# Kernel tuning notes

Measured on AMD Instinct MI355X. Metric: run time of the kernel, lower is better.

The kernel has to match this reference:

```python
import jax, jax.numpy as jnp
import numpy as np

B, F, INP, S = 2048, 50, 2, 1024
LN_EPS = 1e-3
UPDATE_BIAS = -1.0
_TRUNC = 0.8796256610342398  # trunc-normal std correction from weight_init


def _std(fan_in, fan_out):
    return np.sqrt(2.0 / (fan_in + fan_out)) / _TRUNC


def setup_inputs() -> dict:
    key = jax.random.key(0)
    k_act, k_emb, k_gru, k_dec = jax.random.split(key, 4)
    return {
        "action": jax.random.normal(k_act, (B, F, INP), dtype=jnp.float32),
        "W_emb": jax.random.normal(k_emb, (INP, S), dtype=jnp.float32) * _std(INP, S),
        "W_gru": jax.random.normal(k_gru, (2 * S, 3 * S), dtype=jnp.float32) * _std(2 * S, 3 * S),
        "ln_gamma": jnp.ones((3 * S,), dtype=jnp.float32),
        "ln_beta": jnp.zeros((3 * S,), dtype=jnp.float32),
        "W_dec": jax.random.normal(k_dec, (S, INP), dtype=jnp.float32) * _std(S, INP),
        "b_dec": jnp.zeros((INP,), dtype=jnp.float32),
    }


def reference(action, W_emb, W_gru, ln_gamma, ln_beta, W_dec, b_dec):
    # action: [b, f, inp]
    emb = jnp.einsum("bfi,is->bfs", action, W_emb)  # [b, f, s]

    def step(prev, x_t):
        # prev, x_t: [b, s]
        parts = jnp.concatenate([x_t, prev], axis=-1) @ W_gru  # [b, 3s]
        mu = parts.mean(-1, keepdims=True)
        var = parts.var(-1, keepdims=True)
        parts = (parts - mu) / jnp.sqrt(var + LN_EPS) * ln_gamma + ln_beta
        reset, cand, update = jnp.split(parts, 3, axis=-1)
        reset = jax.nn.sigmoid(reset)
        cand = jnp.tanh(reset * cand)
        update = jax.nn.sigmoid(update + UPDATE_BIAS)
        h = update * cand + (1.0 - update) * prev
        return h, None

    prev0 = jnp.zeros_like(emb[:, 0])
    h_last, _ = jax.lax.scan(step, prev0, jnp.swapaxes(emb, 0, 1))  # scan over f
    outputs = h_last @ W_dec + b_dec  # [b, inp]
    return h_last[:, None], outputs[:, None]
```

## Files before the change

kernel.cpp:

```cpp
#include <hip/hip_runtime.h>

typedef unsigned short u16;
typedef unsigned int   u32;
typedef _Float16       f16;

#define B_SZ 2048
#define S_SZ 1024
#define N3   3072
#define F_SZ 50

typedef f16    f16x8 __attribute__((ext_vector_type(8)));
typedef f16    f16x4 __attribute__((ext_vector_type(4)));
typedef float  f32x4 __attribute__((ext_vector_type(4)));
typedef u32    u32x4 __attribute__((ext_vector_type(4)));

__device__ __forceinline__ void glds16(const void* g, void* l) {
    __builtin_amdgcn_global_load_lds(
        (const __attribute__((address_space(1))) u32*)g,
        (__attribute__((address_space(3))) u32*)l, 16, 0, 0);
}

__global__ __launch_bounds__(256) void make_mx(
    const float* __restrict__ We, const float* __restrict__ Wg,
    float* __restrict__ Mx)
{
    int j  = blockIdx.x * 256 + threadIdx.x;
    int k0 = blockIdx.y * 64;
    float s0 = 0.f, s1 = 0.f;
    #pragma unroll 4
    for (int k = k0; k < k0 + 64; k++) {
        float w = Wg[(size_t)k * N3 + j];
        s0 += We[k] * w;
        s1 += We[S_SZ + k] * w;
    }
    atomicAdd(&Mx[j], s0);
    atomicAdd(&Mx[N3 + j], s1);
}

__global__ __launch_bounds__(256) void transpose_w(
    const float* __restrict__ Wg, f16* __restrict__ Wt)
{
    __shared__ float tile[32][33];
    int n0 = blockIdx.x * 32, k0 = blockIdx.y * 32;
    int c = threadIdx.x & 31, r = threadIdx.x >> 5;
    #pragma unroll
    for (int s = 0; s < 4; s++) {
        int rr = r + s * 8;
        tile[rr][c] = Wg[(size_t)(S_SZ + k0 + rr) * N3 + n0 + c];
    }
    __syncthreads();
    #pragma unroll
    for (int s = 0; s < 4; s++) {
        int rr = r + s * 8;
        Wt[(size_t)(n0 + rr) * S_SZ + k0 + c] = (f16)tile[c][rr];
    }
}

__global__ __launch_bounds__(256) void gemm_step(
    const f16* __restrict__ Wt,
    const f16* __restrict__ hh,
    const float* __restrict__ Mx,
    const float* __restrict__ act,
    f16* __restrict__ parts,
    int t, int m_base)
{
    __shared__ __align__(16) f16 As[64 * 64];
    __shared__ __align__(16) f16 Bs[128 * 64];
    const int m0 = m_base + blockIdx.x * 64;
    const int n0 = blockIdx.y * 128;
    const int tid  = threadIdx.x;
    const int lane = tid & 63;
    const int wave = tid >> 6;
    const int wr = (wave >> 1) * 32;
    const int wc = (wave & 1) * 64;
    const int quad = lane >> 4, lrow = lane & 15;
    const int swz = (lrow & 7) * 8;

    const int lrow8 = lane >> 3;
    const int scolh = ((lane & 7) * 8) ^ (lrow8 * 8);

    f32x4 acc[2][4];
    #pragma unroll
    for (int i = 0; i < 2; i++)
        #pragma unroll
        for (int j = 0; j < 4; j++)
            acc[i][j] = (f32x4){0.f, 0.f, 0.f, 0.f};

    for (int kb = 0; kb < S_SZ; kb += 64) {
        __syncthreads();
        #pragma unroll
        for (int c = 0; c < 2; c++) {
            int ch = wave * 2 + c;
            int row = ch * 8 + lrow8;
            glds16(&hh[(size_t)(m0 + row) * S_SZ + kb + scolh], &As[ch * 512]);
        }
        #pragma unroll
        for (int c = 0; c < 4; c++) {
            int ch = wave * 4 + c;
            int row = ch * 8 + lrow8;
            glds16(&Wt[(size_t)(n0 + row) * S_SZ + kb + scolh], &Bs[ch * 512]);
        }
        __syncthreads();
        #pragma unroll
        for (int kk = 0; kk < 64; kk += 32) {
            f16x8 a[2], b[4];
            #pragma unroll
            for (int i = 0; i < 2; i++)
                a[i] = __builtin_bit_cast(f16x8,
                    *(const u32x4*)&As[(wr + i * 16 + lrow) * 64 +
                                       ((kk + quad * 8) ^ swz)]);
            #pragma unroll
            for (int j = 0; j < 4; j++)
                b[j] = __builtin_bit_cast(f16x8,
                    *(const u32x4*)&Bs[(wc + j * 16 + lrow) * 64 +
                                       ((kk + quad * 8) ^ swz)]);
            #pragma unroll
            for (int i = 0; i < 2; i++)
                #pragma unroll
                for (int j = 0; j < 4; j++)
                    acc[i][j] = __builtin_amdgcn_mfma_f32_16x16x32_f16(
                        a[i], b[j], acc[i][j], 0, 0, 0);
        }
    }

    #pragma unroll
    for (int i = 0; i < 2; i++) {
        #pragma unroll
        for (int r = 0; r < 4; r++) {
            int m = m0 + wr + i * 16 + quad * 4 + r;
            float a0 = act[((size_t)m * F_SZ + t) * 2 + 0];
            float a1 = act[((size_t)m * F_SZ + t) * 2 + 1];
            #pragma unroll
            for (int j = 0; j < 4; j++) {
                int n = n0 + wc + j * 16 + lrow;
                parts[(size_t)(m - m_base) * N3 + n] =
                    (f16)(acc[i][j][r] + a0 * Mx[n] + a1 * Mx[N3 + n]);
            }
        }
    }
}

__global__ __launch_bounds__(256) void ln_gate_step(
    const f16* __restrict__ parts,
    const float* __restrict__ gamma,
    const float* __restrict__ beta,
    float* __restrict__ h,
    f16* __restrict__ hh,
    int m_base)
{
    const int rloc = blockIdx.x;
    const int row  = m_base + rloc;
    const int tid  = threadIdx.x;
    const f16* p = parts + (size_t)rloc * N3;
    f16x4 pr = *(const f16x4*)(p + tid * 4);
    f16x4 pc = *(const f16x4*)(p + S_SZ + tid * 4);
    f16x4 pu = *(const f16x4*)(p + 2 * S_SZ + tid * 4);
    float vr[4], vc[4], vu[4];
    float s = 0.f, ss = 0.f;
    #pragma unroll
    for (int q = 0; q < 4; q++) {
        vr[q] = (float)pr[q]; vc[q] = (float)pc[q]; vu[q] = (float)pu[q];
        s  += vr[q] + vc[q] + vu[q];
        ss += vr[q] * vr[q] + vc[q] * vc[q] + vu[q] * vu[q];
    }
    #pragma unroll
    for (int o = 32; o > 0; o >>= 1) {
        s  += __shfl_down(s, o);
        ss += __shfl_down(ss, o);
    }
    __shared__ float red[8];
    int lane = tid & 63, wave = tid >> 6;
    if (lane == 0) { red[wave] = s; red[4 + wave] = ss; }
    __syncthreads();
    float S  = red[0] + red[1] + red[2] + red[3];
    float SS = red[4] + red[5] + red[6] + red[7];
    float mean = S * (1.f / N3);
    float var  = SS * (1.f / N3) - mean * mean;
    float rstd = rsqrtf(var + 1e-3f);

    f32x4 gr = *(const f32x4*)(gamma + tid * 4);
    f32x4 gc = *(const f32x4*)(gamma + S_SZ + tid * 4);
    f32x4 gu = *(const f32x4*)(gamma + 2 * S_SZ + tid * 4);
    f32x4 br = *(const f32x4*)(beta + tid * 4);
    f32x4 bc = *(const f32x4*)(beta + S_SZ + tid * 4);
    f32x4 bu = *(const f32x4*)(beta + 2 * S_SZ + tid * 4);

    size_t hbase = (size_t)row * S_SZ + tid * 4;
    f32x4 hv = *(const f32x4*)(h + hbase);
    f32x4 hn;
    f16x4 hs;
    #pragma unroll
    for (int q = 0; q < 4; q++) {
        float nr = (vr[q] - mean) * rstd * gr[q] + br[q];
        float nc = (vc[q] - mean) * rstd * gc[q] + bc[q];
        float nu = (vu[q] - mean) * rstd * gu[q] + bu[q];
        float r = 1.f / (1.f + __expf(-nr));
        float c = tanhf(r * nc);
        float u = 1.f / (1.f + __expf(-(nu - 1.f)));
        hn[q] = u * c + (1.f - u) * hv[q];
        hs[q] = (f16)hn[q];
    }
    *(f32x4*)(h + hbase) = hn;
    *(f16x4*)(hh + hbase) = hs;
}

__global__ __launch_bounds__(256) void final_out(
    const float* __restrict__ h, const float* __restrict__ Wd,
    const float* __restrict__ bd, float* __restrict__ out)
{
    int row = blockIdx.x * 4 + (threadIdx.x >> 6);
    int lane = threadIdx.x & 63;
    const float* hr = h + (size_t)row * S_SZ;
    float s0 = 0.f, s1 = 0.f;
    #pragma unroll
    for (int k = lane; k < S_SZ; k += 64) {
        float x = hr[k];
        s0 += x * Wd[k * 2];
        s1 += x * Wd[k * 2 + 1];
    }
    #pragma unroll
    for (int o = 32; o > 0; o >>= 1) {
        s0 += __shfl_down(s0, o);
        s1 += __shfl_down(s1, o);
    }
    if (lane == 0) {
        out[(size_t)B_SZ * S_SZ + row * 2 + 0] = s0 + bd[0];
        out[(size_t)B_SZ * S_SZ + row * 2 + 1] = s1 + bd[1];
    }
}

extern "C" void kernel_launch(void* const* d_in, const int* in_sizes, int n_in,
                              void* d_out, int out_size, void* d_ws, size_t ws_size,
                              hipStream_t stream)
{
    const float* act = (const float*)d_in[0];
    const float* We  = (const float*)d_in[1];
    const float* Wg  = (const float*)d_in[2];
    const float* lng = (const float*)d_in[3];
    const float* lnb = (const float*)d_in[4];
    const float* Wd  = (const float*)d_in[5];
    const float* bd  = (const float*)d_in[6];
    float* out = (float*)d_out;
    float* h   = out;

    char* ws = (char*)d_ws;
    f16*   Wt = (f16*)ws;
    float* Mx = (float*)(ws + 6291456);
    f16*   hh = (f16*)(ws + 6316032);
    const size_t BASE = 6316032 + 4194304;
    f16* parts = (f16*)(ws + BASE);
    size_t avail = (ws_size > BASE) ? ws_size - BASE : 0;
    int rows = 2048;
    while (rows > 128 && (size_t)rows * N3 * 2 > avail) rows >>= 1;

    hipMemsetAsync(h, 0, (size_t)B_SZ * S_SZ * 4, stream);
    hipMemsetAsync(hh, 0, (size_t)B_SZ * S_SZ * 2, stream);
    hipMemsetAsync(Mx, 0, 2 * N3 * 4, stream);
    make_mx<<<dim3(N3 / 256, 16), 256, 0, stream>>>(We, Wg, Mx);
    transpose_w<<<dim3(N3 / 32, S_SZ / 32), 256, 0, stream>>>(Wg, Wt);

    for (int t = 0; t < F_SZ; t++) {
        for (int mb = 0; mb < B_SZ; mb += rows) {
            gemm_step<<<dim3(rows / 64, N3 / 128), 256, 0, stream>>>(
                Wt, hh, Mx, act, parts, t, mb);
            ln_gate_step<<<rows, 256, 0, stream>>>(parts, lng, lnb, h, hh, mb);
        }
    }
    final_out<<<B_SZ / 4, 256, 0, stream>>>(h, Wd, bd, out);
}
```

Before: 1.512 ms.

## Fuse GRU time loop into persistent cooperative kernel with per-row-block counters

```diff
diff --git a/kernel.cpp b/kernel.cpp
--- a/kernel.cpp
+++ b/kernel.cpp
@@ -2,17 +2,21 @@
 
 typedef unsigned short u16;
 typedef unsigned int   u32;
+typedef unsigned long long u64;
 typedef _Float16       f16;
 
 #define B_SZ 2048
 #define S_SZ 1024
 #define N3   3072
 #define F_SZ 50
+#define GRID 768
 
 typedef f16    f16x8 __attribute__((ext_vector_type(8)));
 typedef f16    f16x4 __attribute__((ext_vector_type(4)));
 typedef float  f32x4 __attribute__((ext_vector_type(4)));
 typedef u32    u32x4 __attribute__((ext_vector_type(4)));
+
+#define AGENT __HIP_MEMORY_SCOPE_AGENT
 
 __device__ __forceinline__ void glds16(const void* g, void* l) {
     __builtin_amdgcn_global_load_lds(
@@ -56,18 +60,27 @@
     }
 }
 
-__global__ __launch_bounds__(256) void gemm_step(
+__global__ __launch_bounds__(256, 3) void fused_loop(
     const f16* __restrict__ Wt,
-    const f16* __restrict__ hh,
+    f16* __restrict__ hh,
     const float* __restrict__ Mx,
     const float* __restrict__ act,
+    const float* __restrict__ gamma,
+    const float* __restrict__ beta,
     f16* __restrict__ parts,
-    int t, int m_base)
+    float* __restrict__ hout,
+    int* __restrict__ cnt)
 {
     __shared__ __align__(16) f16 As[64 * 64];
     __shared__ __align__(16) f16 Bs[128 * 64];
-    const int m0 = m_base + blockIdx.x * 64;
-    const int n0 = blockIdx.y * 128;
+
+    const int blk = blockIdx.x;
+    const int x8  = blk & 7;
+    const int r   = blk >> 3;
+    const int NB  = x8 * 3 + (r % 3);
+    const int M   = r / 3;
+    const int m0 = M * 64, n0 = NB * 128;
+
     const int tid  = threadIdx.x;
     const int lane = tid & 63;
     const int wave = tid >> 6;
@@ -79,129 +92,185 @@
     const int lrow8 = lane >> 3;
     const int scolh = ((lane & 7) * 8) ^ (lrow8 * 8);
 
-    f32x4 acc[2][4];
-    #pragma unroll
-    for (int i = 0; i < 2; i++)
+    const int arow = tid >> 2;
+    const int agi  = (tid & 3) * 2;
+    const int ar7  = arow & 7;
+
+    const int erow = tid >> 2;
+    const int eseg = (tid & 3) * 32;
+
+    int* gcnt = cnt + M * 16;
+    int* dcnt = cnt + 512 + M * 16;
+    const int doLN = (NB % 3) != 2;
+    const int li   = (NB / 3) * 2 + (NB % 3);
+    const int lnrow = m0 + li * 4 + wave;
+
+    float mx0[4], mx1[4];
+    #pragma unroll
+    for (int j = 0; j < 4; j++) {
+        int n = n0 + wc + j * 16 + lrow;
+        mx0[j] = Mx[n]; mx1[j] = Mx[N3 + n];
+    }
+
+    for (int t = 0; t < F_SZ; t++) {
+        if (tid == 0) {
+            int tgt = 16 * t;
+            while (__hip_atomic_load(dcnt, __ATOMIC_RELAXED, AGENT) < tgt)
+                __builtin_amdgcn_s_sleep(2);
+        }
+        __syncthreads();
+
+        f32x4 acc[2][4];
         #pragma unroll
-        for (int j = 0; j < 4; j++)
-            acc[i][j] = (f32x4){0.f, 0.f, 0.f, 0.f};
-
-    for (int kb = 0; kb < S_SZ; kb += 64) {
+        for (int i = 0; i < 2; i++)
+            #pragma unroll
+            for (int j = 0; j < 4; j++)
+                acc[i][j] = (f32x4){0.f, 0.f, 0.f, 0.f};
+
+        for (int kb = 0; kb < S_SZ; kb += 64) {
+            __syncthreads();
+            {
+                const u64* src = (const u64*)(hh + (size_t)(m0 + arow) * S_SZ + kb)
+                                 + (size_t)(tid & 3) * 4;
+                u64 d0 = __hip_atomic_load(src + 0, __ATOMIC_RELAXED, AGENT);
+                u64 d1 = __hip_atomic_load(src + 1, __ATOMIC_RELAXED, AGENT);
+                u64 d2 = __hip_atomic_load(src + 2, __ATOMIC_RELAXED, AGENT);
+                u64 d3 = __hip_atomic_load(src + 3, __ATOMIC_RELAXED, AGENT);
+                *(u64*)&As[arow * 64 + ((agi    ) ^ ar7) * 8    ] = d0;
+                *(u64*)&As[arow * 64 + ((agi    ) ^ ar7) * 8 + 4] = d1;
+                *(u64*)&As[arow * 64 + ((agi + 1) ^ ar7) * 8    ] = d2;
+                *(u64*)&As[arow * 64 + ((agi + 1) ^ ar7) * 8 + 4] = d3;
+            }
+            #pragma unroll
+            for (int c = 0; c < 4; c++) {
+                int ch = wave * 4 + c;
+                int row = ch * 8 + lrow8;
+                glds16(&Wt[(size_t)(n0 + row) * S_SZ + kb + scolh], &Bs[ch * 512]);
+            }
+            __syncthreads();
+            #pragma unroll
+            for (int kk = 0; kk < 64; kk += 32) {
+                f16x8 a[2], b[4];
+                #pragma unroll
+                for (int i = 0; i < 2; i++)
+                    a[i] = __builtin_bit_cast(f16x8,
+                        *(const u32x4*)&As[(wr + i * 16 + lrow) * 64 +
+                                           ((kk + quad * 8) ^ swz)]);
+                #pragma unroll
+                for (int j = 0; j < 4; j++)
+                    b[j] = __builtin_bit_cast(f16x8,
+                        *(const u32x4*)&Bs[(wc + j * 16 + lrow) * 64 +
+                                           ((kk + quad * 8) ^ swz)]);
+                #pragma unroll
+                for (int i = 0; i < 2; i++)
+                    #pragma unroll
+                    for (int j = 0; j < 4; j++)
+                        acc[i][j] = __builtin_amdgcn_mfma_f32_16x16x32_f16(
+                            a[i], b[j], acc[i][j], 0, 0, 0);
+            }
+        }
+
         __syncthreads();
         #pragma unroll
-        for (int c = 0; c < 2; c++) {
-            int ch = wave * 2 + c;
-            int row = ch * 8 + lrow8;
-            glds16(&hh[(size_t)(m0 + row) * S_SZ + kb + scolh], &As[ch * 512]);
-        }
-        #pragma unroll
-        for (int c = 0; c < 4; c++) {
-            int ch = wave * 4 + c;
-            int row = ch * 8 + lrow8;
-            glds16(&Wt[(size_t)(n0 + row) * S_SZ + kb + scolh], &Bs[ch * 512]);
-        }
-        __syncthreads();
-        #pragma unroll
-        for (int kk = 0; kk < 64; kk += 32) {
-            f16x8 a[2], b[4];
-            #pragma unroll
-            for (int i = 0; i < 2; i++)
-                a[i] = __builtin_bit_cast(f16x8,
-                    *(const u32x4*)&As[(wr + i * 16 + lrow) * 64 +
-                                       ((kk + quad * 8) ^ swz)]);
-            #pragma unroll
-            for (int j = 0; j < 4; j++)
-                b[j] = __builtin_bit_cast(f16x8,
-                    *(const u32x4*)&Bs[(wc + j * 16 + lrow) * 64 +
-                                       ((kk + quad * 8) ^ swz)]);
-            #pragma unroll
-            for (int i = 0; i < 2; i++)
+        for (int i = 0; i < 2; i++) {
+            #pragma unroll
+            for (int rr = 0; rr < 4; rr++) {
+                int mrow = wr + i * 16 + quad * 4 + rr;
+                int m = m0 + mrow;
+                float a0 = act[((size_t)m * F_SZ + t) * 2 + 0];
+                float a1 = act[((size_t)m * F_SZ + t) * 2 + 1];
                 #pragma unroll
                 for (int j = 0; j < 4; j++)
-                    acc[i][j] = __builtin_amdgcn_mfma_f32_16x16x32_f16(
-                        a[i], b[j], acc[i][j], 0, 0, 0);
-        }
-    }
-
-    #pragma unroll
-    for (int i = 0; i < 2; i++) {
-        #pragma unroll
-        for (int r = 0; r < 4; r++) {
-            int m = m0 + wr + i * 16 + quad * 4 + r;
-            float a0 = act[((size_t)m * F_SZ + t) * 2 + 0];
-            float a1 = act[((size_t)m * F_SZ + t) * 2 + 1];
-            #pragma unroll
-            for (int j = 0; j < 4; j++) {
-                int n = n0 + wc + j * 16 + lrow;
-                parts[(size_t)(m - m_base) * N3 + n] =
-                    (f16)(acc[i][j][r] + a0 * Mx[n] + a1 * Mx[N3 + n]);
-            }
-        }
-    }
-}
-
-__global__ __launch_bounds__(256) void ln_gate_step(
-    const f16* __restrict__ parts,
-    const float* __restrict__ gamma,
-    const float* __restrict__ beta,
-    float* __restrict__ h,
-    f16* __restrict__ hh,
-    int m_base)
-{
-    const int rloc = blockIdx.x;
-    const int row  = m_base + rloc;
-    const int tid  = threadIdx.x;
-    const f16* p = parts + (size_t)rloc * N3;
-    f16x4 pr = *(const f16x4*)(p + tid * 4);
-    f16x4 pc = *(const f16x4*)(p + S_SZ + tid * 4);
-    f16x4 pu = *(const f16x4*)(p + 2 * S_SZ + tid * 4);
-    float vr[4], vc[4], vu[4];
-    float s = 0.f, ss = 0.f;
-    #pragma unroll
-    for (int q = 0; q < 4; q++) {
-        vr[q] = (float)pr[q]; vc[q] = (float)pc[q]; vu[q] = (float)pu[q];
-        s  += vr[q] + vc[q] + vu[q];
-        ss += vr[q] * vr[q] + vc[q] * vc[q] + vu[q] * vu[q];
-    }
-    #pragma unroll
-    for (int o = 32; o > 0; o >>= 1) {
-        s  += __shfl_down(s, o);
-        ss += __shfl_down(ss, o);
-    }
-    __shared__ float red[8];
-    int lane = tid & 63, wave = tid >> 6;
-    if (lane == 0) { red[wave] = s; red[4 + wave] = ss; }
-    __syncthreads();
-    float S  = red[0] + red[1] + red[2] + red[3];
-    float SS = red[4] + red[5] + red[6] + red[7];
-    float mean = S * (1.f / N3);
-    float var  = SS * (1.f / N3) - mean * mean;
-    float rstd = rsqrtf(var + 1e-3f);
-
-    f32x4 gr = *(const f32x4*)(gamma + tid * 4);
-    f32x4 gc = *(const f32x4*)(gamma + S_SZ + tid * 4);
-    f32x4 gu = *(const f32x4*)(gamma + 2 * S_SZ + tid * 4);
-    f32x4 br = *(const f32x4*)(beta + tid * 4);
-    f32x4 bc = *(const f32x4*)(beta + S_SZ + tid * 4);
-    f32x4 bu = *(const f32x4*)(beta + 2 * S_SZ + tid * 4);
-
-    size_t hbase = (size_t)row * S_SZ + tid * 4;
-    f32x4 hv = *(const f32x4*)(h + hbase);
-    f32x4 hn;
-    f16x4 hs;
-    #pragma unroll
-    for (int q = 0; q < 4; q++) {
-        float nr = (vr[q] - mean) * rstd * gr[q] + br[q];
-        float nc = (vc[q] - mean) * rstd * gc[q] + bc[q];
-        float nu = (vu[q] - mean) * rstd * gu[q] + bu[q];
-        float r = 1.f / (1.f + __expf(-nr));
-        float c = tanhf(r * nc);
-        float u = 1.f / (1.f + __expf(-(nu - 1.f)));
-        hn[q] = u * c + (1.f - u) * hv[q];
-        hs[q] = (f16)hn[q];
-    }
-    *(f32x4*)(h + hbase) = hn;
-    *(f16x4*)(hh + hbase) = hs;
+                    Bs[mrow * 128 + wc + j * 16 + lrow] =
+                        (f16)(acc[i][j][rr] + a0 * mx0[j] + a1 * mx1[j]);
+            }
+        }
+        __syncthreads();
+        {
+            u64* dst = (u64*)(parts + (size_t)(m0 + erow) * N3 + n0 + eseg);
+            const u64* srcl = (const u64*)&Bs[erow * 128 + eseg];
+            #pragma unroll
+            for (int e = 0; e < 8; e++)
+                __hip_atomic_store(dst + e, srcl[e], __ATOMIC_RELAXED, AGENT);
+        }
+        __syncthreads();
+        if (tid == 0)
+            __hip_atomic_fetch_add(gcnt, 1, __ATOMIC_RELEASE, AGENT);
+
+        if (tid == 0) {
+            int tgt = 24 * (t + 1);
+            while (__hip_atomic_load(gcnt, __ATOMIC_RELAXED, AGENT) < tgt)
+                __builtin_amdgcn_s_sleep(2);
+        }
+        __syncthreads();
+
+        if (doLN) {
+            const int row = lnrow;
+            const f16* prow = parts + (size_t)row * N3;
+            const int l = lane;
+            float v[48];
+            float s = 0.f, ss = 0.f;
+            #pragma unroll
+            for (int gte = 0; gte < 3; gte++) {
+                #pragma unroll
+                for (int q = 0; q < 4; q++) {
+                    u64 raw = __hip_atomic_load(
+                        (const u64*)(prow + gte * S_SZ + q * 256 + l * 4),
+                        __ATOMIC_RELAXED, AGENT);
+                    f16x4 xv = __builtin_bit_cast(f16x4, raw);
+                    #pragma unroll
+                    for (int e = 0; e < 4; e++) {
+                        float f = (float)xv[e];
+                        v[gte * 16 + q * 4 + e] = f;
+                        s += f; ss += f * f;
+                    }
+                }
+            }
+            #pragma unroll
+            for (int o = 1; o < 64; o <<= 1) {
+                s  += __shfl_xor(s, o);
+                ss += __shfl_xor(ss, o);
+            }
+            float mean = s * (1.f / N3);
+            float var  = ss * (1.f / N3) - mean * mean;
+            float rstd = rsqrtf(var + 1e-3f);
+            #pragma unroll
+            for (int q = 0; q < 4; q++) {
+                int off = q * 256 + l * 4;
+                f32x4 gr = *(const f32x4*)(gamma + off);
+                f32x4 gc = *(const f32x4*)(gamma + S_SZ + off);
+                f32x4 gu = *(const f32x4*)(gamma + 2 * S_SZ + off);
+                f32x4 br = *(const f32x4*)(beta + off);
+                f32x4 bc = *(const f32x4*)(beta + S_SZ + off);
+                f32x4 bu = *(const f32x4*)(beta + 2 * S_SZ + off);
+                u64 rawp = __hip_atomic_load(
+                    (const u64*)(hh + (size_t)row * S_SZ + off),
+                    __ATOMIC_RELAXED, AGENT);
+                f16x4 hp4 = __builtin_bit_cast(f16x4, rawp);
+                f32x4 hn; f16x4 hs;
+                #pragma unroll
+                for (int e = 0; e < 4; e++) {
+                    int k = q * 4 + e;
+                    float nr = (v[k]      - mean) * rstd * gr[e] + br[e];
+                    float nc = (v[16 + k] - mean) * rstd * gc[e] + bc[e];
+                    float nu = (v[32 + k] - mean) * rstd * gu[e] + bu[e];
+                    float rg = 1.f / (1.f + __expf(-nr));
+                    float cg = tanhf(rg * nc);
+                    float ug = 1.f / (1.f + __expf(-(nu - 1.f)));
+                    float hv = ug * cg + (1.f - ug) * (float)hp4[e];
+                    hn[e] = hv; hs[e] = (f16)hv;
+                }
+                __hip_atomic_store((u64*)(hh + (size_t)row * S_SZ + off),
+                                   __builtin_bit_cast(u64, hs),
+                                   __ATOMIC_RELAXED, AGENT);
+                if (t == F_SZ - 1)
+                    *(f32x4*)(hout + (size_t)row * S_SZ + off) = hn;
+            }
+        }
+        __syncthreads();
+        if (doLN && tid == 0)
+            __hip_atomic_fetch_add(dcnt, 1, __ATOMIC_RELEASE, AGENT);
+    }
 }
 
 __global__ __launch_bounds__(256) void final_out(
@@ -241,30 +310,28 @@
     const float* Wd  = (const float*)d_in[5];
     const float* bd  = (const float*)d_in[6];
     float* out = (float*)d_out;
-    float* h   = out;
 
     char* ws = (char*)d_ws;
-    f16*   Wt = (f16*)ws;
-    float* Mx = (float*)(ws + 6291456);
-    f16*   hh = (f16*)(ws + 6316032);
-    const size_t BASE = 6316032 + 4194304;
-    f16* parts = (f16*)(ws + BASE);
-    size_t avail = (ws_size > BASE) ? ws_size - BASE : 0;
-    int rows = 2048;
-    while (rows > 128 && (size_t)rows * N3 * 2 > avail) rows >>= 1;
-
-    hipMemsetAsync(h, 0, (size_t)B_SZ * S_SZ * 4, stream);
+    f16*   Wt    = (f16*)ws;
+    float* Mx    = (float*)(ws + 6291456);
+    f16*   hh    = (f16*)(ws + 6316032);
+    f16*   parts = (f16*)(ws + 10510336);
+    int*   cnt   = (int*)(ws + 23093248);
+
     hipMemsetAsync(hh, 0, (size_t)B_SZ * S_SZ * 2, stream);
     hipMemsetAsync(Mx, 0, 2 * N3 * 4, stream);
+    hipMemsetAsync(cnt, 0, 4096, stream);
     make_mx<<<dim3(N3 / 256, 16), 256, 0, stream>>>(We, Wg, Mx);
     transpose_w<<<dim3(N3 / 32, S_SZ / 32), 256, 0, stream>>>(Wg, Wt);
 
-    for (int t = 0; t < F_SZ; t++) {
-        for (int mb = 0; mb < B_SZ; mb += rows) {
-            gemm_step<<<dim3(rows / 64, N3 / 128), 256, 0, stream>>>(
-                Wt, hh, Mx, act, parts, t, mb);
-            ln_gate_step<<<rows, 256, 0, stream>>>(parts, lng, lnb, h, hh, mb);
-        }
-    }
-    final_out<<<B_SZ / 4, 256, 0, stream>>>(h, Wd, bd, out);
-}
+    void* kargs[] = {(void*)&Wt, (void*)&hh, (void*)&Mx, (void*)&act,
+                     (void*)&lng, (void*)&lnb, (void*)&parts, (void*)&out,
+                     (void*)&cnt};
+    hipError_t e = hipLaunchCooperativeKernel((void*)fused_loop, dim3(GRID),
+                                              dim3(256), kargs, 0, stream);
+    if (e != hipSuccess)
+        fused_loop<<<GRID, 256, 0, stream>>>(
+            Wt, hh, Mx, act, lng, lnb, parts, out, cnt);
+
+    final_out<<<B_SZ / 4, 256, 0, stream>>>(out, Wd, bd, out);
+}
```

Result: slower. 4.184 ms (+176.8%).

## Deepen GEMM K-tile, remap blocks, and drop fp32 hidden state from the step loop

Applied to the files above, without the earlier changes.

```diff
diff --git a/kernel.cpp b/kernel.cpp
--- a/kernel.cpp
+++ b/kernel.cpp
@@ -2,6 +2,7 @@
 
 typedef unsigned short u16;
 typedef unsigned int   u32;
+typedef unsigned long long u64;
 typedef _Float16       f16;
 
 #define B_SZ 2048
@@ -56,28 +57,34 @@
     }
 }
 
-__global__ __launch_bounds__(256) void gemm_step(
+__global__ __launch_bounds__(256, 3) void gemm_step(
     const f16* __restrict__ Wt,
     const f16* __restrict__ hh,
     const float* __restrict__ Mx,
     const float* __restrict__ act,
     f16* __restrict__ parts,
-    int t, int m_base)
-{
-    __shared__ __align__(16) f16 As[64 * 64];
-    __shared__ __align__(16) f16 Bs[128 * 64];
-    const int m0 = m_base + blockIdx.x * 64;
-    const int n0 = blockIdx.y * 128;
+    int t)
+{
+    __shared__ __align__(16) f16 As[64 * 128];
+    __shared__ __align__(16) f16 Bs[128 * 128];
+
+    const int blk = blockIdx.x;
+    const int x8  = blk & 7;
+    const int r   = blk >> 3;
+    const int NB  = x8 * 3 + (r % 3);
+    const int M   = r / 3;
+    const int m0 = M * 64, n0 = NB * 128;
+
     const int tid  = threadIdx.x;
     const int lane = tid & 63;
     const int wave = tid >> 6;
     const int wr = (wave >> 1) * 32;
     const int wc = (wave & 1) * 64;
     const int quad = lane >> 4, lrow = lane & 15;
-    const int swz = (lrow & 7) * 8;
-
-    const int lrow8 = lane >> 3;
-    const int scolh = ((lane & 7) * 8) ^ (lrow8 * 8);
+    const int lr7 = lrow & 7;
+
+    const int srow = lane >> 4;
+    const int sgrn = (lane & 15);
 
     f32x4 acc[2][4];
     #pragma unroll
@@ -86,34 +93,37 @@
         for (int j = 0; j < 4; j++)
             acc[i][j] = (f32x4){0.f, 0.f, 0.f, 0.f};
 
-    for (int kb = 0; kb < S_SZ; kb += 64) {
+    for (int kb = 0; kb < S_SZ; kb += 128) {
         __syncthreads();
-        #pragma unroll
-        for (int c = 0; c < 2; c++) {
-            int ch = wave * 2 + c;
-            int row = ch * 8 + lrow8;
-            glds16(&hh[(size_t)(m0 + row) * S_SZ + kb + scolh], &As[ch * 512]);
-        }
         #pragma unroll
         for (int c = 0; c < 4; c++) {
             int ch = wave * 4 + c;
-            int row = ch * 8 + lrow8;
-            glds16(&Wt[(size_t)(n0 + row) * S_SZ + kb + scolh], &Bs[ch * 512]);
+            int row = ch * 4 + srow;
+            int g = sgrn ^ (row & 7);
+            glds16(&hh[(size_t)(m0 + row) * S_SZ + kb + g * 8], &As[ch * 512]);
+        }
+        #pragma unroll
+        for (int c = 0; c < 8; c++) {
+            int ch = wave * 8 + c;
+            int row = ch * 4 + srow;
+            int g = sgrn ^ (row & 7);
+            glds16(&Wt[(size_t)(n0 + row) * S_SZ + kb + g * 8], &Bs[ch * 512]);
         }
         __syncthreads();
         #pragma unroll
-        for (int kk = 0; kk < 64; kk += 32) {
+        for (int kk = 0; kk < 128; kk += 32) {
             f16x8 a[2], b[4];
+            int gq = (kk >> 3) + quad;
             #pragma unroll
             for (int i = 0; i < 2; i++)
                 a[i] = __builtin_bit_cast(f16x8,
-                    *(const u32x4*)&As[(wr + i * 16 + lrow) * 64 +
-                                       ((kk + quad * 8) ^ swz)]);
+                    *(const u32x4*)&As[(wr + i * 16 + lrow) * 128 +
+                                       (gq ^ lr7) * 8]);
             #pragma unroll
             for (int j = 0; j < 4; j++)
                 b[j] = __builtin_bit_cast(f16x8,
-                    *(const u32x4*)&Bs[(wc + j * 16 + lrow) * 64 +
-                                       ((kk + quad * 8) ^ swz)]);
+                    *(const u32x4*)&Bs[(wc + j * 16 + lrow) * 128 +
+                                       (gq ^ lr7) * 8]);
             #pragma unroll
             for (int i = 0; i < 2; i++)
                 #pragma unroll
@@ -126,15 +136,15 @@
     #pragma unroll
     for (int i = 0; i < 2; i++) {
         #pragma unroll
-        for (int r = 0; r < 4; r++) {
-            int m = m0 + wr + i * 16 + quad * 4 + r;
+        for (int rr = 0; rr < 4; rr++) {
+            int m = m0 + wr + i * 16 + quad * 4 + rr;
             float a0 = act[((size_t)m * F_SZ + t) * 2 + 0];
             float a1 = act[((size_t)m * F_SZ + t) * 2 + 1];
             #pragma unroll
             for (int j = 0; j < 4; j++) {
                 int n = n0 + wc + j * 16 + lrow;
-                parts[(size_t)(m - m_base) * N3 + n] =
-                    (f16)(acc[i][j][r] + a0 * Mx[n] + a1 * Mx[N3 + n]);
+                parts[(size_t)m * N3 + n] =
+                    (f16)(acc[i][j][rr] + a0 * Mx[n] + a1 * Mx[N3 + n]);
             }
         }
     }
@@ -144,64 +154,75 @@
     const f16* __restrict__ parts,
     const float* __restrict__ gamma,
     const float* __restrict__ beta,
-    float* __restrict__ h,
     f16* __restrict__ hh,
-    int m_base)
-{
-    const int rloc = blockIdx.x;
-    const int row  = m_base + rloc;
-    const int tid  = threadIdx.x;
-    const f16* p = parts + (size_t)rloc * N3;
-    f16x4 pr = *(const f16x4*)(p + tid * 4);
-    f16x4 pc = *(const f16x4*)(p + S_SZ + tid * 4);
-    f16x4 pu = *(const f16x4*)(p + 2 * S_SZ + tid * 4);
-    float vr[4], vc[4], vu[4];
+    float* __restrict__ hout,
+    int t)
+{
+    const int tid = threadIdx.x;
+    const int r2  = tid >> 7;
+    const int tl  = tid & 127;
+    const int row = blockIdx.x * 2 + r2;
+    const f16* p = parts + (size_t)row * N3 + tl * 8;
+
+    float v[24];
     float s = 0.f, ss = 0.f;
     #pragma unroll
-    for (int q = 0; q < 4; q++) {
-        vr[q] = (float)pr[q]; vc[q] = (float)pc[q]; vu[q] = (float)pu[q];
-        s  += vr[q] + vc[q] + vu[q];
-        ss += vr[q] * vr[q] + vc[q] * vc[q] + vu[q] * vu[q];
-    }
-    #pragma unroll
-    for (int o = 32; o > 0; o >>= 1) {
-        s  += __shfl_down(s, o);
-        ss += __shfl_down(ss, o);
+    for (int g = 0; g < 3; g++) {
+        f16x8 x = *(const f16x8*)(p + g * S_SZ);
+        #pragma unroll
+        for (int e = 0; e < 8; e++) {
+            float f = (float)x[e];
+            v[g * 8 + e] = f;
+            s += f; ss += f * f;
+        }
+    }
+    #pragma unroll
+    for (int o = 1; o < 64; o <<= 1) {
+        s  += __shfl_xor(s, o);
+        ss += __shfl_xor(ss, o);
     }
     __shared__ float red[8];
-    int lane = tid & 63, wave = tid >> 6;
+    int wave = tid >> 6, lane = tid & 63;
     if (lane == 0) { red[wave] = s; red[4 + wave] = ss; }
     __syncthreads();
-    float S  = red[0] + red[1] + red[2] + red[3];
-    float SS = red[4] + red[5] + red[6] + red[7];
+    float S  = red[r2 * 2] + red[r2 * 2 + 1];
+    float SS = red[4 + r2 * 2] + red[4 + r2 * 2 + 1];
     float mean = S * (1.f / N3);
     float var  = SS * (1.f / N3) - mean * mean;
     float rstd = rsqrtf(var + 1e-3f);
 
-    f32x4 gr = *(const f32x4*)(gamma + tid * 4);
-    f32x4 gc = *(const f32x4*)(gamma + S_SZ + tid * 4);
-    f32x4 gu = *(const f32x4*)(gamma + 2 * S_SZ + tid * 4);
-    f32x4 br = *(const f32x4*)(beta + tid * 4);
-    f32x4 bc = *(const f32x4*)(beta + S_SZ + tid * 4);
-    f32x4 bu = *(const f32x4*)(beta + 2 * S_SZ + tid * 4);
-
-    size_t hbase = (size_t)row * S_SZ + tid * 4;
-    f32x4 hv = *(const f32x4*)(h + hbase);
-    f32x4 hn;
-    f16x4 hs;
-    #pragma unroll
-    for (int q = 0; q < 4; q++) {
-        float nr = (vr[q] - mean) * rstd * gr[q] + br[q];
-        float nc = (vc[q] - mean) * rstd * gc[q] + bc[q];
-        float nu = (vu[q] - mean) * rstd * gu[q] + bu[q];
-        float r = 1.f / (1.f + __expf(-nr));
-        float c = tanhf(r * nc);
-        float u = 1.f / (1.f + __expf(-(nu - 1.f)));
-        hn[q] = u * c + (1.f - u) * hv[q];
-        hs[q] = (f16)hn[q];
-    }
-    *(f32x4*)(h + hbase) = hn;
-    *(f16x4*)(hh + hbase) = hs;
+    float nv[24];
+    #pragma unroll
+    for (int g = 0; g < 3; g++) {
+        f32x4 g0 = *(const f32x4*)(gamma + g * S_SZ + tl * 8);
+        f32x4 g1 = *(const f32x4*)(gamma + g * S_SZ + tl * 8 + 4);
+        f32x4 b0 = *(const f32x4*)(beta  + g * S_SZ + tl * 8);
+        f32x4 b1 = *(const f32x4*)(beta  + g * S_SZ + tl * 8 + 4);
+        #pragma unroll
+        for (int e = 0; e < 4; e++) {
+            nv[g * 8 + e]     = (v[g * 8 + e]     - mean) * rstd * g0[e] + b0[e];
+            nv[g * 8 + e + 4] = (v[g * 8 + e + 4] - mean) * rstd * g1[e] + b1[e];
+        }
+    }
+
+    size_t hbase = (size_t)row * S_SZ + tl * 8;
+    f16x8 hp = *(const f16x8*)(hh + hbase);
+    f16x8 hs;
+    f32x4 ho0, ho1;
+    #pragma unroll
+    for (int e = 0; e < 8; e++) {
+        float rg = 1.f / (1.f + __expf(-nv[e]));
+        float cg = tanhf(rg * nv[8 + e]);
+        float ug = 1.f / (1.f + __expf(-(nv[16 + e] - 1.f)));
+        float hv = ug * cg + (1.f - ug) * (float)hp[e];
+        hs[e] = (f16)hv;
+        if (e < 4) ho0[e] = hv; else ho1[e - 4] = hv;
+    }
+    *(f16x8*)(hh + hbase) = hs;
+    if (t == F_SZ - 1) {
+        *(f32x4*)(hout + hbase)     = ho0;
+        *(f32x4*)(hout + hbase + 4) = ho1;
+    }
 }
 
 __global__ __launch_bounds__(256) void final_out(
@@ -241,30 +262,21 @@
     const float* Wd  = (const float*)d_in[5];
     const float* bd  = (const float*)d_in[6];
     float* out = (float*)d_out;
-    float* h   = out;
 
     char* ws = (char*)d_ws;
-    f16*   Wt = (f16*)ws;
-    float* Mx = (float*)(ws + 6291456);
-    f16*   hh = (f16*)(ws + 6316032);
-    const size_t BASE = 6316032 + 4194304;
-    f16* parts = (f16*)(ws + BASE);
-    size_t avail = (ws_size > BASE) ? ws_size - BASE : 0;
-    int rows = 2048;
-    while (rows > 128 && (size_t)rows * N3 * 2 > avail) rows >>= 1;
-
-    hipMemsetAsync(h, 0, (size_t)B_SZ * S_SZ * 4, stream);
+    f16*   Wt    = (f16*)ws;
+    float* Mx    = (float*)(ws + 6291456);
+    f16*   hh    = (f16*)(ws + 6316032);
+    f16*   parts = (f16*)(ws + 10510336);
+
     hipMemsetAsync(hh, 0, (size_t)B_SZ * S_SZ * 2, stream);
     hipMemsetAsync(Mx, 0, 2 * N3 * 4, stream);
     make_mx<<<dim3(N3 / 256, 16), 256, 0, stream>>>(We, Wg, Mx);
     transpose_w<<<dim3(N3 / 32, S_SZ / 32), 256, 0, stream>>>(Wg, Wt);
 
     for (int t = 0; t < F_SZ; t++) {
-        for (int mb = 0; mb < B_SZ; mb += rows) {
-            gemm_step<<<dim3(rows / 64, N3 / 128), 256, 0, stream>>>(
-                Wt, hh, Mx, act, parts, t, mb);
-            ln_gate_step<<<rows, 256, 0, stream>>>(parts, lng, lnb, h, hh, mb);
-        }
-    }
-    final_out<<<B_SZ / 4, 256, 0, stream>>>(h, Wd, bd, out);
-}
+        gemm_step<<<768, 256, 0, stream>>>(Wt, hh, Mx, act, parts, t);
+        ln_gate_step<<<B_SZ / 2, 256, 0, stream>>>(parts, lng, lnb, hh, out, t);
+    }
+    final_out<<<B_SZ / 4, 256, 0, stream>>>(out, Wd, bd, out);
+}
```

Measured after the change: 1.678 ms. +11.0%, slower.
